# Kernel tuning notes

Hardware: AMD Instinct MI355X
Metric: run time of the kernel (lower is better)

The kernel has to match this reference:

```python
import jax, jax.numpy as jnp
import numpy as np

EMBED_DIM = 512
NUM_HEADS = 8
N_WIRES = 8  # kernel uses only first N_WIRES dims of each head vector


def setup_inputs() -> dict:
    key = jax.random.key(0)
    x = jax.random.normal(key, (8, 1024, EMBED_DIM), dtype=jnp.float32)
    return {"x": x}


def reference(x):
    B, S, E = x.shape
    H = NUM_HEADS
    dk = E // H
    # [B, H, S, dk]
    xh = x.reshape(B, S, H, dk).transpose(0, 2, 1, 3)
    # Quantum RY-overlap kernel closed form:
    #   RY(-y) RY(x) |0> = RY(x - y) |0>  =>  <0...0|psi> = prod_w cos((x_w - y_w)/2)
    # Only the first N_WIRES components of each head vector are used
    # (states.view(-1)[0] reads the first batch row's |0..0> amplitude).
    xw = xh[..., :N_WIRES]  # [B, H, S, NW]
    scores = jnp.ones((B, H, S, S), dtype=x.dtype)
    for w in range(N_WIRES):  # fixed small loop, fuses under jit
        diff = xw[:, :, :, None, w] - xw[:, :, None, :, w]  # [B, H, S, S]
        scores = scores * jnp.cos(diff * 0.5)
    scores = jnp.abs(scores)
    attn = jax.nn.softmax(scores, axis=-1)  # dropout is identity at eval
    out = jnp.einsum("bhij,bhjd->bhid", attn, xh)  # [B, H, S, dk]
    return out.transpose(0, 2, 1, 3).reshape(B, S, E)
```

## Files before the change

kernel.cpp:

```cpp
#include <hip/hip_runtime.h>

#define B_  8
#define S_  1024
#define E_  512
#define TI  128
#define TJ  32
#define P_STR 40
#define V_STR 40

typedef _Float16 half_t;
typedef _Float16 half4_t __attribute__((ext_vector_type(4)));
typedef _Float16 half8_t __attribute__((ext_vector_type(8)));
typedef float    floatx16 __attribute__((ext_vector_type(16)));

__device__ __forceinline__ void make_frags(float4 w0, float4 w1, int hf,
                                           half8_t* fH, half8_t* fL) {
    float xi[8] = {w0.x, w0.y, w0.z, w0.w, w1.x, w1.y, w1.z, w1.w};
    float c[8], s[8];
    #pragma unroll
    for (int w = 0; w < 8; ++w) {
        float v = xi[w] * 0.5f;
        c[w] = __cosf(v);
        s[w] = __sinf(v);
    }
    float p01[4] = {c[0]*c[1], s[0]*c[1], c[0]*s[1], s[0]*s[1]};
    float p23[4] = {c[2]*c[3], s[2]*c[3], c[2]*s[3], s[2]*s[3]};
    float p45[4] = {c[4]*c[5], s[4]*c[5], c[4]*s[5], s[4]*s[5]};
    float p67[4] = {c[6]*c[7], s[6]*c[7], c[6]*s[7], s[6]*s[7]};
    #pragma unroll
    for (int idx = 0; idx < 8; ++idx) {
        int a = idx & 3;
        int bsel = (idx >> 2) | (hf << 1);
        (*fL)[idx] = (half_t)(p01[a] * p23[bsel]);
        (*fH)[idx] = (half_t)(p45[a] * p67[bsel]);
    }
}

__global__ __launch_bounds__(256, 2) void attn_kernel(const float* __restrict__ x,
                                                      float* __restrict__ out) {
    const int bh = blockIdx.x;
    const int b  = bh >> 3, h = bh & 7;
    const int i0 = blockIdx.y * TI;
    const int t  = threadIdx.x;
    const int wv = t >> 6;
    const int ln = t & 63;
    const int m  = ln & 31;
    const int hf = ln >> 5;
    const int lo = t & 7;

    __shared__ __align__(16) half_t sh_p[TI * P_STR];
    __shared__ __align__(16) half_t sh_v[64 * V_STR];
    __shared__ float sh_den[TI];

    const float* xh = x + (size_t)b * S_ * E_ + h * 64;

    half8_t biH, biL;
    {
        const float* px = xh + (size_t)(i0 + wv * 32 + m) * E_;
        float4 w0 = ((const float4*)px)[0];
        float4 w1 = ((const float4*)px)[1];
        make_frags(w0, w1, hf, &biH, &biL);
    }

    floatx16 acc0, acc1, z;
    #pragma unroll
    for (int k = 0; k < 16; ++k) { acc0[k] = 0.f; acc1[k] = 0.f; z[k] = 0.f; }
    float dacc = 0.f;

    const int sv_j  = t >> 3;
    const int sv_d0 = lo * 8;

    for (int j0 = 0; j0 < S_; j0 += TJ) {
        __syncthreads();

        const float* pj = xh + (size_t)(j0 + m) * E_;
        float4 jw0 = ((const float4*)pj)[0];
        float4 jw1 = ((const float4*)pj)[1];
        const float* pv = xh + (size_t)(j0 + sv_j) * E_ + sv_d0;
        float4 v0 = ((const float4*)pv)[0];
        float4 v1 = ((const float4*)pv)[1];

        half8_t ajH, ajL;
        make_frags(jw0, jw1, hf, &ajH, &ajL);

        {
            float vals[8] = {v0.x, v0.y, v0.z, v0.w, v1.x, v1.y, v1.z, v1.w};
            #pragma unroll
            for (int nq = 0; nq < 8; ++nq) {
                int q = (nq + lo) & 7;
                sh_v[(sv_d0 + q) * V_STR + sv_j] = (half_t)vals[q];
            }
        }
        __syncthreads();

        floatx16 sH = __builtin_amdgcn_mfma_f32_32x32x16_f16(ajH, biH, z, 0, 0, 0);
        floatx16 sL = __builtin_amdgcn_mfma_f32_32x32x16_f16(ajL, biL, z, 0, 0, 0);

        const int irow = wv * 32 + m;
        #pragma unroll
        for (int g = 0; g < 4; ++g) {
            half4_t pk;
            #pragma unroll
            for (int r = 0; r < 4; ++r) {
                float sc = sH[4 * g + r] * sL[4 * g + r];
                float p = __expf(__builtin_fabsf(sc));
                dacc += p;
                pk[r] = (half_t)p;
            }
            *(half4_t*)&sh_p[irow * P_STR + g * 8 + hf * 4] = pk;
        }

        const half_t* prow = &sh_p[(wv * 32 + m) * P_STR];
        half8_t ap0 = *(const half8_t*)(prow + hf * 8);
        half8_t ap1 = *(const half8_t*)(prow + 16 + hf * 8);
        const half_t* vr0 = &sh_v[m * V_STR];
        const half_t* vr1 = &sh_v[(32 + m) * V_STR];
        half8_t b00 = *(const half8_t*)(vr0 + hf * 8);
        half8_t b01 = *(const half8_t*)(vr0 + 16 + hf * 8);
        half8_t b10 = *(const half8_t*)(vr1 + hf * 8);
        half8_t b11 = *(const half8_t*)(vr1 + 16 + hf * 8);
        acc0 = __builtin_amdgcn_mfma_f32_32x32x16_f16(ap0, b00, acc0, 0, 0, 0);
        acc0 = __builtin_amdgcn_mfma_f32_32x32x16_f16(ap1, b01, acc0, 0, 0, 0);
        acc1 = __builtin_amdgcn_mfma_f32_32x32x16_f16(ap0, b10, acc1, 0, 0, 0);
        acc1 = __builtin_amdgcn_mfma_f32_32x32x16_f16(ap1, b11, acc1, 0, 0, 0);
    }

    dacc += __shfl_xor(dacc, 32, 64);
    sh_den[wv * 32 + m] = dacc;
    __syncthreads();

    #pragma unroll
    for (int reg = 0; reg < 16; ++reg) {
        int il = (reg & 3) + 8 * (reg >> 2) + 4 * hf;
        float inv = 1.f / sh_den[wv * 32 + il];
        size_t base = ((size_t)(b * S_ + i0 + wv * 32 + il)) * E_ + h * 64 + m;
        out[base]      = acc0[reg] * inv;
        out[base + 32] = acc1[reg] * inv;
    }
}

extern "C" void kernel_launch(void* const* d_in, const int* in_sizes, int n_in,
                              void* d_out, int out_size, void* d_ws, size_t ws_size,
                              hipStream_t stream) {
    const float* x = (const float*)d_in[0];
    float* out = (float*)d_out;
    attn_kernel<<<dim3(B_ * 8, S_ / TI), 256, 0, stream>>>(x, out);
}
```

Measured before the change: 111.7 us.

## Precompute phi features and transposed fp16 V in workspace prepasses

Adds two prepass kernels. One computes the per-row trigonometric product features (phi) once and stores them as fp16. The other writes a transposed fp16 copy of V to workspace. The attention kernel then loads these directly from global memory with register double-buffering and no per-iteration syncthreads, so each j-tile no longer recomputes the features or restages V through LDS. The cost is two extra launches and workspace traffic, and the original kernel is kept as a fallback when workspace is too small.

```diff
diff --git a/kernel.cpp b/kernel.cpp
--- a/kernel.cpp
+++ b/kernel.cpp
@@ -6,15 +6,20 @@
 #define TI  128
 #define TJ  32
 #define P_STR 40
-#define V_STR 40
 
 typedef _Float16 half_t;
 typedef _Float16 half4_t __attribute__((ext_vector_type(4)));
 typedef _Float16 half8_t __attribute__((ext_vector_type(8)));
 typedef float    floatx16 __attribute__((ext_vector_type(16)));
 
-__device__ __forceinline__ void make_frags(float4 w0, float4 w1, int hf,
-                                           half8_t* fH, half8_t* fL) {
+__global__ __launch_bounds__(256) void phi_kernel(const float* __restrict__ x,
+                                                  half_t* __restrict__ phi) {
+    int idx = blockIdx.x * 256 + threadIdx.x;
+    int bh = idx >> 10, j = idx & 1023;
+    int b = bh >> 3, h = bh & 7;
+    const float* px = x + ((size_t)(b * S_ + j)) * E_ + h * 64;
+    float4 w0 = ((const float4*)px)[0];
+    float4 w1 = ((const float4*)px)[1];
     float xi[8] = {w0.x, w0.y, w0.z, w0.w, w1.x, w1.y, w1.z, w1.w};
     float c[8], s[8];
     #pragma unroll
@@ -27,17 +32,44 @@
     float p23[4] = {c[2]*c[3], s[2]*c[3], c[2]*s[3], s[2]*s[3]};
     float p45[4] = {c[4]*c[5], s[4]*c[5], c[4]*s[5], s[4]*s[5]};
     float p67[4] = {c[6]*c[7], s[6]*c[7], c[6]*s[7], s[6]*s[7]};
-    #pragma unroll
-    for (int idx = 0; idx < 8; ++idx) {
-        int a = idx & 3;
-        int bsel = (idx >> 2) | (hf << 1);
-        (*fL)[idx] = (half_t)(p01[a] * p23[bsel]);
-        (*fH)[idx] = (half_t)(p45[a] * p67[bsel]);
-    }
-}
-
-__global__ __launch_bounds__(256, 2) void attn_kernel(const float* __restrict__ x,
-                                                      float* __restrict__ out) {
+    half_t o[32];
+    #pragma unroll
+    for (int kk = 0; kk < 16; ++kk) {
+        o[kk]      = (half_t)(p01[kk & 3] * p23[kk >> 2]);
+        o[16 + kk] = (half_t)(p45[kk & 3] * p67[kk >> 2]);
+    }
+    half8_t* dst = (half8_t*)(phi + (size_t)idx * 32);
+    dst[0] = *(half8_t*)&o[0];
+    dst[1] = *(half8_t*)&o[8];
+    dst[2] = *(half8_t*)&o[16];
+    dst[3] = *(half8_t*)&o[24];
+}
+
+__global__ __launch_bounds__(256) void vt_kernel(const float* __restrict__ x,
+                                                 half_t* __restrict__ vt) {
+    int bh = blockIdx.x >> 5, j0 = (blockIdx.x & 31) * 32;
+    int b = bh >> 3, h = bh & 7;
+    int t = threadIdx.x;
+    __shared__ half_t sh[64 * P_STR];
+    int jj = t >> 3, lo = t & 7, d0 = lo * 8;
+    const float* src = x + ((size_t)(b * S_ + j0 + jj)) * E_ + h * 64 + d0;
+    float4 a = ((const float4*)src)[0];
+    float4 cc = ((const float4*)src)[1];
+    float vals[8] = {a.x, a.y, a.z, a.w, cc.x, cc.y, cc.z, cc.w};
+    #pragma unroll
+    for (int nq = 0; nq < 8; ++nq) {
+        int q = (nq + lo) & 7;
+        sh[(d0 + q) * P_STR + jj] = (half_t)vals[q];
+    }
+    __syncthreads();
+    int d = t >> 2, seg = t & 3;
+    half8_t v = *(half8_t*)&sh[d * P_STR + seg * 8];
+    *(half8_t*)(vt + ((size_t)(bh * 64 + d)) * 1024 + j0 + seg * 8) = v;
+}
+
+__global__ __launch_bounds__(256, 2) void attn_phi_kernel(const half_t* __restrict__ phi,
+                                                          const half_t* __restrict__ vt,
+                                                          float* __restrict__ out) {
     const int bh = blockIdx.x;
     const int b  = bh >> 3, h = bh & 7;
     const int i0 = blockIdx.y * TI;
@@ -46,56 +78,154 @@
     const int ln = t & 63;
     const int m  = ln & 31;
     const int hf = ln >> 5;
-    const int lo = t & 7;
 
     __shared__ __align__(16) half_t sh_p[TI * P_STR];
-    __shared__ __align__(16) half_t sh_v[64 * V_STR];
     __shared__ float sh_den[TI];
 
+    const half_t* phibh = phi + (size_t)bh * (1024 * 32);
+    const half_t* vtbh  = vt  + (size_t)bh * (64 * 1024);
+
+    const half_t* pi = phibh + (size_t)(i0 + wv * 32 + m) * 32 + hf * 8;
+    half8_t biL = *(const half8_t*)pi;
+    half8_t biH = *(const half8_t*)(pi + 16);
+
+    floatx16 acc0, acc1, z;
+    #pragma unroll
+    for (int k = 0; k < 16; ++k) { acc0[k] = 0.f; acc1[k] = 0.f; z[k] = 0.f; }
+    float dacc0 = 0.f, dacc1 = 0.f;
+
+    const int irow = wv * 32 + m;
+    const half_t* prow = &sh_p[irow * P_STR];
+
+    const half_t* pj  = phibh + (size_t)m * 32 + hf * 8;
+    const half_t* v0p = vtbh + (size_t)m * 1024 + hf * 8;
+    const half_t* v1p = vtbh + (size_t)(32 + m) * 1024 + hf * 8;
+    half8_t ajL = *(const half8_t*)pj;
+    half8_t ajH = *(const half8_t*)(pj + 16);
+    half8_t b00 = *(const half8_t*)v0p;
+    half8_t b01 = *(const half8_t*)(v0p + 16);
+    half8_t b10 = *(const half8_t*)v1p;
+    half8_t b11 = *(const half8_t*)(v1p + 16);
+
+    for (int j0 = 0; j0 < S_; j0 += TJ) {
+        int jn = (j0 + TJ) & (S_ - 1);
+        const half_t* pjn  = phibh + (size_t)(jn + m) * 32 + hf * 8;
+        const half_t* v0pn = vtbh + (size_t)m * 1024 + jn + hf * 8;
+        const half_t* v1pn = vtbh + (size_t)(32 + m) * 1024 + jn + hf * 8;
+        half8_t najL = *(const half8_t*)pjn;
+        half8_t najH = *(const half8_t*)(pjn + 16);
+        half8_t nb00 = *(const half8_t*)v0pn;
+        half8_t nb01 = *(const half8_t*)(v0pn + 16);
+        half8_t nb10 = *(const half8_t*)v1pn;
+        half8_t nb11 = *(const half8_t*)(v1pn + 16);
+
+        floatx16 sH = __builtin_amdgcn_mfma_f32_32x32x16_f16(ajH, biH, z, 0, 0, 0);
+        floatx16 sL = __builtin_amdgcn_mfma_f32_32x32x16_f16(ajL, biL, z, 0, 0, 0);
+
+        #pragma unroll
+        for (int g = 0; g < 4; ++g) {
+            half4_t pk;
+            #pragma unroll
+            for (int r = 0; r < 4; ++r) {
+                float sc = sH[4 * g + r] * sL[4 * g + r];
+                float p = __expf(__builtin_fabsf(sc));
+                if (r & 1) dacc1 += p; else dacc0 += p;
+                pk[r] = (half_t)p;
+            }
+            *(half4_t*)&sh_p[irow * P_STR + g * 8 + hf * 4] = pk;
+        }
+
+        half8_t ap0 = *(const half8_t*)(prow + hf * 8);
+        half8_t ap1 = *(const half8_t*)(prow + 16 + hf * 8);
+        acc0 = __builtin_amdgcn_mfma_f32_32x32x16_f16(ap0, b00, acc0, 0, 0, 0);
+        acc0 = __builtin_amdgcn_mfma_f32_32x32x16_f16(ap1, b01, acc0, 0, 0, 0);
+        acc1 = __builtin_amdgcn_mfma_f32_32x32x16_f16(ap0, b10, acc1, 0, 0, 0);
+        acc1 = __builtin_amdgcn_mfma_f32_32x32x16_f16(ap1, b11, acc1, 0, 0, 0);
+
+        ajL = najL; ajH = najH;
+        b00 = nb00; b01 = nb01; b10 = nb10; b11 = nb11;
+    }
+
+    float dacc = dacc0 + dacc1;
+    dacc += __shfl_xor(dacc, 32, 64);
+    sh_den[wv * 32 + m] = dacc;
+    __syncthreads();
+
+    #pragma unroll
+    for (int reg = 0; reg < 16; ++reg) {
+        int il = (reg & 3) + 8 * (reg >> 2) + 4 * hf;
+        float inv = 1.f / sh_den[wv * 32 + il];
+        size_t base = ((size_t)(b * S_ + i0 + wv * 32 + il)) * E_ + h * 64 + m;
+        out[base]      = acc0[reg] * inv;
+        out[base + 32] = acc1[reg] * inv;
+    }
+}
+
+__device__ __forceinline__ void make_frags_fb(float4 w0, float4 w1, int hf,
+                                              half8_t* fH, half8_t* fL) {
+    float xi[8] = {w0.x, w0.y, w0.z, w0.w, w1.x, w1.y, w1.z, w1.w};
+    float c[8], s[8];
+    #pragma unroll
+    for (int w = 0; w < 8; ++w) {
+        float v = xi[w] * 0.5f;
+        c[w] = __cosf(v);
+        s[w] = __sinf(v);
+    }
+    float p01[4] = {c[0]*c[1], s[0]*c[1], c[0]*s[1], s[0]*s[1]};
+    float p23[4] = {c[2]*c[3], s[2]*c[3], c[2]*s[3], s[2]*s[3]};
+    float p45[4] = {c[4]*c[5], s[4]*c[5], c[4]*s[5], s[4]*s[5]};
+    float p67[4] = {c[6]*c[7], s[6]*c[7], c[6]*s[7], s[6]*s[7]};
+    #pragma unroll
+    for (int idx = 0; idx < 8; ++idx) {
+        int a = idx & 3;
+        int bsel = (idx >> 2) | (hf << 1);
+        (*fL)[idx] = (half_t)(p01[a] * p23[bsel]);
+        (*fH)[idx] = (half_t)(p45[a] * p67[bsel]);
+    }
+}
+
+__global__ __launch_bounds__(256, 2) void attn_fb_kernel(const float* __restrict__ x,
+                                                         float* __restrict__ out) {
+    const int bh = blockIdx.x;
+    const int b  = bh >> 3, h = bh & 7;
+    const int i0 = blockIdx.y * TI;
+    const int t  = threadIdx.x;
+    const int wv = t >> 6, ln = t & 63, m = ln & 31, hf = ln >> 5, lo = t & 7;
+    __shared__ __align__(16) half_t sh_p[TI * P_STR];
+    __shared__ __align__(16) half_t sh_v[64 * P_STR];
+    __shared__ float sh_den[TI];
     const float* xh = x + (size_t)b * S_ * E_ + h * 64;
-
     half8_t biH, biL;
     {
         const float* px = xh + (size_t)(i0 + wv * 32 + m) * E_;
-        float4 w0 = ((const float4*)px)[0];
-        float4 w1 = ((const float4*)px)[1];
-        make_frags(w0, w1, hf, &biH, &biL);
-    }
-
+        make_frags_fb(((const float4*)px)[0], ((const float4*)px)[1], hf, &biH, &biL);
+    }
     floatx16 acc0, acc1, z;
     #pragma unroll
     for (int k = 0; k < 16; ++k) { acc0[k] = 0.f; acc1[k] = 0.f; z[k] = 0.f; }
     float dacc = 0.f;
-
-    const int sv_j  = t >> 3;
-    const int sv_d0 = lo * 8;
-
+    const int sv_j = t >> 3, sv_d0 = lo * 8;
     for (int j0 = 0; j0 < S_; j0 += TJ) {
         __syncthreads();
-
-        const float* pj = xh + (size_t)(j0 + m) * E_;
-        float4 jw0 = ((const float4*)pj)[0];
-        float4 jw1 = ((const float4*)pj)[1];
+        const float* pjx = xh + (size_t)(j0 + m) * E_;
+        float4 jw0 = ((const float4*)pjx)[0];
+        float4 jw1 = ((const float4*)pjx)[1];
         const float* pv = xh + (size_t)(j0 + sv_j) * E_ + sv_d0;
         float4 v0 = ((const float4*)pv)[0];
         float4 v1 = ((const float4*)pv)[1];
-
         half8_t ajH, ajL;
-        make_frags(jw0, jw1, hf, &ajH, &ajL);
-
+        make_frags_fb(jw0, jw1, hf, &ajH, &ajL);
         {
             float vals[8] = {v0.x, v0.y, v0.z, v0.w, v1.x, v1.y, v1.z, v1.w};
             #pragma unroll
             for (int nq = 0; nq < 8; ++nq) {
                 int q = (nq + lo) & 7;
-                sh_v[(sv_d0 + q) * V_STR + sv_j] = (half_t)vals[q];
+                sh_v[(sv_d0 + q) * P_STR + sv_j] = (half_t)vals[q];
             }
         }
         __syncthreads();
-
         floatx16 sH = __builtin_amdgcn_mfma_f32_32x32x16_f16(ajH, biH, z, 0, 0, 0);
         floatx16 sL = __builtin_amdgcn_mfma_f32_32x32x16_f16(ajL, biL, z, 0, 0, 0);
-
         const int irow = wv * 32 + m;
         #pragma unroll
         for (int g = 0; g < 4; ++g) {
@@ -109,12 +239,11 @@
             }
             *(half4_t*)&sh_p[irow * P_STR + g * 8 + hf * 4] = pk;
         }
-
         const half_t* prow = &sh_p[(wv * 32 + m) * P_STR];
         half8_t ap0 = *(const half8_t*)(prow + hf * 8);
         half8_t ap1 = *(const half8_t*)(prow + 16 + hf * 8);
-        const half_t* vr0 = &sh_v[m * V_STR];
-        const half_t* vr1 = &sh_v[(32 + m) * V_STR];
+        const half_t* vr0 = &sh_v[m * P_STR];
+        const half_t* vr1 = &sh_v[(32 + m) * P_STR];
         half8_t b00 = *(const half8_t*)(vr0 + hf * 8);
         half8_t b01 = *(const half8_t*)(vr0 + 16 + hf * 8);
         half8_t b10 = *(const half8_t*)(vr1 + hf * 8);
@@ -124,11 +253,9 @@
         acc1 = __builtin_amdgcn_mfma_f32_32x32x16_f16(ap0, b10, acc1, 0, 0, 0);
         acc1 = __builtin_amdgcn_mfma_f32_32x32x16_f16(ap1, b11, acc1, 0, 0, 0);
     }
-
     dacc += __shfl_xor(dacc, 32, 64);
     sh_den[wv * 32 + m] = dacc;
     __syncthreads();
-
     #pragma unroll
     for (int reg = 0; reg < 16; ++reg) {
         int il = (reg & 3) + 8 * (reg >> 2) + 4 * hf;
@@ -144,5 +271,15 @@
                               hipStream_t stream) {
     const float* x = (const float*)d_in[0];
     float* out = (float*)d_out;
-    attn_kernel<<<dim3(B_ * 8, S_ / TI), 256, 0, stream>>>(x, out);
-}
+    const size_t PHI_BYTES = (size_t)64 * 1024 * 32 * sizeof(half_t);
+    const size_t VT_BYTES  = (size_t)64 * 64 * 1024 * sizeof(half_t);
+    if (ws_size >= PHI_BYTES + VT_BYTES) {
+        half_t* phi = (half_t*)d_ws;
+        half_t* vt  = (half_t*)((char*)d_ws + PHI_BYTES);
+        phi_kernel<<<dim3(64 * 1024 / 256), 256, 0, stream>>>(x, phi);
+        vt_kernel<<<dim3(64 * 32), 256, 0, stream>>>(x, vt);
+        attn_phi_kernel<<<dim3(B_ * 8, S_ / TI), 256, 0, stream>>>(phi, vt, out);
+    } else {
+        attn_fb_kernel<<<dim3(B_ * 8, S_ / TI), 256, 0, stream>>>(x, out);
+    }
+}
```

Result: no change. 112.3 us (+0.5%).
